# Kernel tuning notes

Hardware: AMD Instinct MI355X
Metric: run time of the kernel (lower is better)

## Reference

```python
import jax, jax.numpy as jnp
import numpy as np

N_FFT = 2048
HOP = 512


def _hann(n):
    # scipy.signal.get_window('hann', n, fftbins=True)
    return (0.5 - 0.5 * np.cos(2.0 * np.pi * np.arange(n) / n)).astype(np.float32)


def setup_inputs() -> dict:
    key = jax.random.key(0)
    k1, k2 = jax.random.split(key)
    B, T, F = 8, 1000, N_FFT // 2 + 1
    real_stft = jax.random.normal(k1, (B, 1, T, F), dtype=jnp.float32)
    imag_stft = jax.random.normal(k2, (B, 1, T, F), dtype=jnp.float32)

    # Windowed IDFT matrices, exactly as ISTFT.__init__ builds conv weights.
    n = N_FFT
    x, y = np.meshgrid(np.arange(n), np.arange(n))
    ang = 2.0 * np.pi * ((x * y) % n) / n  # angle of omega**(x*y), omega = exp(2*pi*i/n)
    win = _hann(n)  # win_length == n_fft -> pad_center is a no-op
    W_real = (np.cos(ang) / n * win[:, None]).astype(np.float32)
    W_imag = (np.sin(ang) / n * win[:, None]).astype(np.float32)

    return {
        "real_stft": real_stft,
        "imag_stft": imag_stft,
        "W_real": jnp.asarray(W_real),
        "W_imag": jnp.asarray(W_imag),
        "window": jnp.asarray(win),
        "length": 511488,  # HOP * (n_frames - 1) with n_frames = 1000
    }


def reference(real_stft, imag_stft, W_real, W_imag, window, length):
    n_fft, hop = N_FFT, HOP
    B = real_stft.shape[0]

    fr = jnp.swapaxes(real_stft[:, 0], 1, 2)  # (B, n_fft//2+1, T)
    fi = jnp.swapaxes(imag_stft[:, 0], 1, 2)
    # Hermitian symmetry -> full (B, n_fft, T) spectrum
    full_r = jnp.concatenate([fr, jnp.flip(fr[:, 1:-1, :], axis=1)], axis=1)
    full_i = jnp.concatenate([fi, -jnp.flip(fi[:, 1:-1, :], axis=1)], axis=1)

    # center=True and length given (static Python int)
    padded_length = length + n_fft
    n_frames = min(fr.shape[2], -(-padded_length // hop))

    # windowed real IFFT per frame: s[b, o, t]
    s = (jnp.einsum('oi,bit->bot', W_real, full_r[:, :, :n_frames])
         - jnp.einsum('oi,bit->bot', W_imag, full_i[:, :, :n_frames]))

    L = n_fft + hop * (n_frames - 1)
    # fused overlap-add via scatter-add
    idx = (jnp.arange(n_frames)[:, None] * hop + jnp.arange(n_fft)[None, :]).reshape(-1)
    frames = jnp.swapaxes(s, 1, 2).reshape(B, -1)  # (B, n_frames*n_fft)
    y = jnp.zeros((B, L), s.dtype).at[:, idx].add(frames)

    # window sum-square normalization (librosa.filters.window_sumsquare)
    wss = jnp.zeros((L,), window.dtype).at[idx].add(jnp.tile(window ** 2, n_frames))
    tiny = jnp.finfo(window.dtype).tiny
    nz = wss > tiny
    y = jnp.where(nz[None, :], y / jnp.where(nz, wss, 1.0)[None, :], y)

    start = n_fft // 2
    return y[:, start:start + length]
```

## Files before the change

### kernel.cpp

```cpp
#include <hip/hip_runtime.h>


#define N_FFT    2048
#define HOP      512
#define T_FRAMES 1000
#define F_BINS   1025
#define OUT_LEN  511488

#define P(a) ((a) + ((a) >> 4))

__device__ __forceinline__ void cmul(float ar, float ai, float br, float bi,
                                     float& cr, float& ci) {
    cr = ar * br - ai * bi;
    ci = ar * bi + ai * br;
}

__device__ __forceinline__ unsigned short f2bf(float f) {
    union { float f; unsigned int u; } v; v.f = f;
    unsigned int u = v.u;
    u += 0x7fffu + ((u >> 16) & 1u);
    return (unsigned short)(u >> 16);
}

__device__ __forceinline__ float bf2f(unsigned short h) {
    union { unsigned int u; float f; } v;
    v.u = ((unsigned int)h) << 16;
    return v.f;
}

__global__ __launch_bounds__(256) void istft_fft_kernel(const float* __restrict__ re,
                                                        const float* __restrict__ im,
                                                        const float* __restrict__ win,
                                                        unsigned short* __restrict__ S) {
    __shared__ float2 buf[1088];

    const int f   = blockIdx.x;
    const int tid = threadIdx.x;
    const float* fr = re + (size_t)f * F_BINS;
    const float* fi = im + (size_t)f * F_BINS;

    const float Sc = 0.5f / 1024.f;
    #pragma unroll
    for (int k0 = 0; k0 < 1024; k0 += 256) {
        int k = k0 + tid;
        float ar = fr[k];
        float ai = (k == 0) ? 0.f : fi[k];
        int mk = 1024 - k;
        float br = fr[mk];
        float bi = (mk == 1024) ? 0.f : fi[mk];
        float dr = ar - br, di = ai + bi;
        float ang = 3.14159265358979f * (float)k / 1024.f;
        float sn, cs;
        __sincosf(ang, &sn, &cs);
        float Zr = (ar + br - (cs * di + sn * dr)) * Sc;
        float Zi = (ai - bi + (cs * dr - sn * di)) * Sc;
        unsigned r10 = __brev((unsigned)k) >> 22;
        int rk = (int)(((r10 & 0x155u) << 1) | ((r10 >> 1) & 0x155u));
        buf[P(rk)] = make_float2(Zr, Zi);
    }
    __syncthreads();

    {
        int base = tid << 2;
        int i0 = P(base), i1 = P(base + 1), i2 = P(base + 2), i3 = P(base + 3);
        float2 a = buf[i0], b = buf[i1], c = buf[i2], d = buf[i3];
        float t0r = a.x + c.x, t0i = a.y + c.y;
        float t1r = a.x - c.x, t1i = a.y - c.y;
        float t2r = b.x + d.x, t2i = b.y + d.y;
        float t3r = b.x - d.x, t3i = b.y - d.y;
        buf[i0] = make_float2(t0r + t2r, t0i + t2i);
        buf[i1] = make_float2(t1r - t3i, t1i + t3r);
        buf[i2] = make_float2(t0r - t2r, t0i - t2i);
        buf[i3] = make_float2(t1r + t3i, t1i - t3r);
    }

    #pragma unroll
    for (int s = 1; s < 4; ++s) {
        __builtin_amdgcn_wave_barrier();
        const int hm = 1 << (2 * s);
        const int j    = tid & (hm - 1);
        const int base = ((tid - j) << 2) + j;
        float ang = 1.57079632679f * (float)j / (float)hm;
        float s1, c1;
        __sincosf(ang, &s1, &c1);
        float c2, s2, c3, s3;
        cmul(c1, s1, c1, s1, c2, s2);
        cmul(c2, s2, c1, s1, c3, s3);

        int i0 = P(base), i1 = P(base + hm), i2 = P(base + 2 * hm), i3 = P(base + 3 * hm);
        float2 a = buf[i0], b = buf[i1], c = buf[i2], d = buf[i3];
        float br_, bi_, cr_, ci_, dr_, di_;
        cmul(b.x, b.y, c1, s1, br_, bi_);
        cmul(c.x, c.y, c2, s2, cr_, ci_);
        cmul(d.x, d.y, c3, s3, dr_, di_);

        float t0r = a.x + cr_, t0i = a.y + ci_;
        float t1r = a.x - cr_, t1i = a.y - ci_;
        float t2r = br_ + dr_, t2i = bi_ + di_;
        float t3r = br_ - dr_, t3i = bi_ - di_;
        buf[i0] = make_float2(t0r + t2r, t0i + t2i);
        buf[i1] = make_float2(t1r - t3i, t1i + t3r);
        buf[i2] = make_float2(t0r - t2r, t0i - t2i);
        buf[i3] = make_float2(t1r + t3i, t1i - t3r);
    }
    __syncthreads();

    {
        unsigned int* dst = (unsigned int*)(S + (size_t)f * N_FFT);
        const float2* w2v = (const float2*)win;

        float ang = 1.57079632679f * (float)tid / 256.f;
        float s1, c1;
        __sincosf(ang, &s1, &c1);
        float c2, s2, c3, s3;
        cmul(c1, s1, c1, s1, c2, s2);
        cmul(c2, s2, c1, s1, c3, s3);

        int i0 = P(tid), i1 = P(tid + 256), i2 = P(tid + 512), i3 = P(tid + 768);
        float2 a = buf[i0], b = buf[i1], c = buf[i2], d = buf[i3];
        float br_, bi_, cr_, ci_, dr_, di_;
        cmul(b.x, b.y, c1, s1, br_, bi_);
        cmul(c.x, c.y, c2, s2, cr_, ci_);
        cmul(d.x, d.y, c3, s3, dr_, di_);

        float t0r = a.x + cr_, t0i = a.y + ci_;
        float t1r = a.x - cr_, t1i = a.y - ci_;
        float t2r = br_ + dr_, t2i = bi_ + di_;
        float t3r = br_ - dr_, t3i = bi_ - di_;

        float2 z0 = make_float2(t0r + t2r, t0i + t2i);
        float2 z1 = make_float2(t1r - t3i, t1i + t3r);
        float2 z2 = make_float2(t0r - t2r, t0i - t2i);
        float2 z3 = make_float2(t1r + t3i, t1i - t3r);

        float2 w0 = w2v[tid],       w1 = w2v[tid + 256];
        float2 w2 = w2v[tid + 512], w3 = w2v[tid + 768];
        dst[tid]       = (unsigned int)f2bf(z0.x * w0.x) | ((unsigned int)f2bf(z0.y * w0.y) << 16);
        dst[tid + 256] = (unsigned int)f2bf(z1.x * w1.x) | ((unsigned int)f2bf(z1.y * w1.y) << 16);
        dst[tid + 512] = (unsigned int)f2bf(z2.x * w2.x) | ((unsigned int)f2bf(z2.y * w2.y) << 16);
        dst[tid + 768] = (unsigned int)f2bf(z3.x * w3.x) | ((unsigned int)f2bf(z3.y * w3.y) << 16);
    }
}

__global__ __launch_bounds__(256) void norm_kernel(const unsigned short* __restrict__ S,
                                                   const float* __restrict__ win,
                                                   float* __restrict__ out) {
    const int b  = blockIdx.y;
    const int m0 = (blockIdx.x * 256 + threadIdx.x) * 8;

    if (blockIdx.x >= 1 && blockIdx.x <= 248) {
        const int n0  = m0 + N_FFT / 2;
        const int thi = n0 >> 9;
        const int r   = n0 & 511;

        float acc[8] = {0.f, 0.f, 0.f, 0.f, 0.f, 0.f, 0.f, 0.f};
        #pragma unroll
        for (int kk = 0; kk < 4; ++kk) {
            const int t = thi - kk;
            const int o = r + (kk << 9);
            const uint4 v = *reinterpret_cast<const uint4*>(
                S + ((size_t)(b * T_FRAMES + t)) * N_FFT + o);
            const unsigned int u[4] = {v.x, v.y, v.z, v.w};
            #pragma unroll
            for (int q = 0; q < 4; ++q) {
                union { unsigned int u32; float f; } lo, hi;
                lo.u32 = u[q] << 16;
                hi.u32 = u[q] & 0xffff0000u;
                acc[2 * q]     += lo.f;
                acc[2 * q + 1] += hi.f;
            }
        }
        const float inv = 1.f / 1.5f;
        float* o_ptr = out + (size_t)b * OUT_LEN + m0;
        float4 v0 = make_float4(acc[0] * inv, acc[1] * inv, acc[2] * inv, acc[3] * inv);
        float4 v1 = make_float4(acc[4] * inv, acc[5] * inv, acc[6] * inv, acc[7] * inv);
        reinterpret_cast<float4*>(o_ptr)[0] = v0;
        reinterpret_cast<float4*>(o_ptr)[1] = v1;
    } else {
        for (int e = 0; e < 8; ++e) {
            int m = m0 + e;
            if (m >= OUT_LEN) continue;
            int n = m + N_FFT / 2;
            int thi = n >> 9; if (thi > T_FRAMES - 1) thi = T_FRAMES - 1;
            int tlo = (n - (N_FFT - HOP)) >> 9; if (tlo < 0) tlo = 0;

            float sum = 0.f, wss = 0.f;
            for (int t = tlo; t <= thi; ++t) {
                int o = n - (t << 9);
                sum += bf2f(S[((size_t)(b * T_FRAMES + t)) * N_FFT + o]);
                float w = win[o];
                wss += w * w;
            }
            out[(size_t)b * OUT_LEN + m] = (wss > 1.17549435e-38f) ? sum / wss : sum;
        }
    }
}

extern "C" void kernel_launch(void* const* d_in, const int* in_sizes, int n_in,
                              void* d_out, int out_size, void* d_ws, size_t ws_size,
                              hipStream_t stream) {
    const float* re  = (const float*)d_in[0];
    const float* im  = (const float*)d_in[1];
    const float* win = (const float*)d_in[4];
    float* out = (float*)d_out;

    unsigned short* S = (unsigned short*)d_ws;

    istft_fft_kernel<<<8000, 256, 0, stream>>>(re, im, win, S);
    norm_kernel<<<dim3(250, 8), 256, 0, stream>>>(S, win, out);
}
```

Baseline: 146.1 us.

## Fuse per-frame IFFT with shared-memory overlap-add and handle block seams separately

Each block now processes eight consecutive frames of one batch item. It accumulates their windowed IFFT outputs in shared memory and writes interior output samples directly, already normalized. Only the overlapping edge regions go to a small fp32 scratch buffer, which a seam kernel sums and normalizes, including the boundary window-sum-square handling. This removes the large bf16 intermediate frame buffer and its global write and read-back. The cost is far fewer blocks, 1000 instead of 8000, with frames handled serially inside each block and extra barriers, so less latency hiding.

```diff
diff --git a/kernel.cpp b/kernel.cpp
--- a/kernel.cpp
+++ b/kernel.cpp
@@ -6,6 +6,9 @@
 #define T_FRAMES 1000
 #define F_BINS   1025
 #define OUT_LEN  511488
+#define FPB      8
+#define BPB      125
+#define OAF      5632
 
 #define P(a) ((a) + ((a) >> 4))
 
@@ -15,184 +18,198 @@
     ci = ar * bi + ai * br;
 }
 
-__device__ __forceinline__ unsigned short f2bf(float f) {
-    union { float f; unsigned int u; } v; v.f = f;
-    unsigned int u = v.u;
-    u += 0x7fffu + ((u >> 16) & 1u);
-    return (unsigned short)(u >> 16);
-}
-
-__device__ __forceinline__ float bf2f(unsigned short h) {
-    union { unsigned int u; float f; } v;
-    v.u = ((unsigned int)h) << 16;
-    return v.f;
-}
-
-__global__ __launch_bounds__(256) void istft_fft_kernel(const float* __restrict__ re,
-                                                        const float* __restrict__ im,
-                                                        const float* __restrict__ win,
-                                                        unsigned short* __restrict__ S) {
-    __shared__ float2 buf[1088];
-
-    const int f   = blockIdx.x;
+__global__ __launch_bounds__(256) void istft_oa_kernel(const float* __restrict__ re,
+                                                       const float* __restrict__ im,
+                                                       const float* __restrict__ win,
+                                                       float* __restrict__ scratch,
+                                                       float* __restrict__ out) {
+    __shared__ __align__(16) float2 buf[1088];
+    __shared__ __align__(16) float2 oa2[OAF / 2];
+
+    const int j   = blockIdx.x;
+    const int b   = blockIdx.y;
     const int tid = threadIdx.x;
-    const float* fr = re + (size_t)f * F_BINS;
-    const float* fi = im + (size_t)f * F_BINS;
+    const int t0  = j * FPB;
+
+    {
+        float4* z4 = (float4*)oa2;
+        #pragma unroll
+        for (int e = 0; e < 6; ++e) {
+            int idx = tid + 256 * e;
+            if (idx < 1408) z4[idx] = make_float4(0.f, 0.f, 0.f, 0.f);
+        }
+    }
 
     const float Sc = 0.5f / 1024.f;
+    const float2* w2v = (const float2*)win;
+
+    for (int d = 0; d < FPB; ++d) {
+        const int f = b * T_FRAMES + t0 + d;
+        const float* fr = re + (size_t)f * F_BINS;
+        const float* fi = im + (size_t)f * F_BINS;
+
+        #pragma unroll
+        for (int k0 = 0; k0 < 1024; k0 += 256) {
+            int k = k0 + tid;
+            float ar = fr[k];
+            float ai = (k == 0) ? 0.f : fi[k];
+            int mk = 1024 - k;
+            float br = fr[mk];
+            float bi = (mk == 1024) ? 0.f : fi[mk];
+            float dr = ar - br, di = ai + bi;
+            float ang = 3.14159265358979f * (float)k / 1024.f;
+            float sn, cs;
+            __sincosf(ang, &sn, &cs);
+            float Zr = (ar + br - (cs * di + sn * dr)) * Sc;
+            float Zi = (ai - bi + (cs * dr - sn * di)) * Sc;
+            unsigned r10 = __brev((unsigned)k) >> 22;
+            int rk = (int)(((r10 & 0x155u) << 1) | ((r10 >> 1) & 0x155u));
+            buf[P(rk)] = make_float2(Zr, Zi);
+        }
+        __syncthreads();
+
+        {
+            int base = tid << 2;
+            int i0 = P(base), i1 = P(base + 1), i2 = P(base + 2), i3 = P(base + 3);
+            float2 a = buf[i0], bb = buf[i1], c = buf[i2], dd = buf[i3];
+            float t0r = a.x + c.x,  t0i = a.y + c.y;
+            float t1r = a.x - c.x,  t1i = a.y - c.y;
+            float t2r = bb.x + dd.x, t2i = bb.y + dd.y;
+            float t3r = bb.x - dd.x, t3i = bb.y - dd.y;
+            buf[i0] = make_float2(t0r + t2r, t0i + t2i);
+            buf[i1] = make_float2(t1r - t3i, t1i + t3r);
+            buf[i2] = make_float2(t0r - t2r, t0i - t2i);
+            buf[i3] = make_float2(t1r + t3i, t1i - t3r);
+        }
+
+        #pragma unroll
+        for (int s = 1; s < 4; ++s) {
+            __builtin_amdgcn_wave_barrier();
+            const int hm = 1 << (2 * s);
+            const int jj   = tid & (hm - 1);
+            const int base = ((tid - jj) << 2) + jj;
+            float ang = 1.57079632679f * (float)jj / (float)hm;
+            float s1, c1;
+            __sincosf(ang, &s1, &c1);
+            float c2, s2, c3, s3;
+            cmul(c1, s1, c1, s1, c2, s2);
+            cmul(c2, s2, c1, s1, c3, s3);
+
+            int i0 = P(base), i1 = P(base + hm), i2 = P(base + 2 * hm), i3 = P(base + 3 * hm);
+            float2 a = buf[i0], bb = buf[i1], c = buf[i2], dd = buf[i3];
+            float br_, bi_, cr_, ci_, dr_, di_;
+            cmul(bb.x, bb.y, c1, s1, br_, bi_);
+            cmul(c.x,  c.y,  c2, s2, cr_, ci_);
+            cmul(dd.x, dd.y, c3, s3, dr_, di_);
+
+            float t0r = a.x + cr_, t0i = a.y + ci_;
+            float t1r = a.x - cr_, t1i = a.y - ci_;
+            float t2r = br_ + dr_, t2i = bi_ + di_;
+            float t3r = br_ - dr_, t3i = bi_ - di_;
+            buf[i0] = make_float2(t0r + t2r, t0i + t2i);
+            buf[i1] = make_float2(t1r - t3i, t1i + t3r);
+            buf[i2] = make_float2(t0r - t2r, t0i - t2i);
+            buf[i3] = make_float2(t1r + t3i, t1i - t3r);
+        }
+        __syncthreads();
+
+        {
+            float ang = 1.57079632679f * (float)tid / 256.f;
+            float s1, c1;
+            __sincosf(ang, &s1, &c1);
+            float c2, s2, c3, s3;
+            cmul(c1, s1, c1, s1, c2, s2);
+            cmul(c2, s2, c1, s1, c3, s3);
+
+            int i0 = P(tid), i1 = P(tid + 256), i2 = P(tid + 512), i3 = P(tid + 768);
+            float2 a = buf[i0], bb = buf[i1], c = buf[i2], dd = buf[i3];
+            float br_, bi_, cr_, ci_, dr_, di_;
+            cmul(bb.x, bb.y, c1, s1, br_, bi_);
+            cmul(c.x,  c.y,  c2, s2, cr_, ci_);
+            cmul(dd.x, dd.y, c3, s3, dr_, di_);
+
+            float t0r = a.x + cr_, t0i = a.y + ci_;
+            float t1r = a.x - cr_, t1i = a.y - ci_;
+            float t2r = br_ + dr_, t2i = bi_ + di_;
+            float t3r = br_ - dr_, t3i = bi_ - di_;
+
+            float2 z0 = make_float2(t0r + t2r, t0i + t2i);
+            float2 z1 = make_float2(t1r - t3i, t1i + t3r);
+            float2 z2 = make_float2(t0r - t2r, t0i - t2i);
+            float2 z3 = make_float2(t1r + t3i, t1i - t3r);
+
+            float2 w0 = w2v[tid],       w1 = w2v[tid + 256];
+            float2 w2 = w2v[tid + 512], w3 = w2v[tid + 768];
+
+            const int base2 = 256 * d;
+            float2 v;
+            v = oa2[base2 + tid];
+            v.x += z0.x * w0.x;  v.y += z0.y * w0.y;
+            oa2[base2 + tid] = v;
+            v = oa2[base2 + tid + 256];
+            v.x += z1.x * w1.x;  v.y += z1.y * w1.y;
+            oa2[base2 + tid + 256] = v;
+            v = oa2[base2 + tid + 512];
+            v.x += z2.x * w2.x;  v.y += z2.y * w2.y;
+            oa2[base2 + tid + 512] = v;
+            v = oa2[base2 + tid + 768];
+            v.x += z3.x * w3.x;  v.y += z3.y * w3.y;
+            oa2[base2 + tid + 768] = v;
+        }
+        __syncthreads();
+    }
+
+    const float inv = 2.f / 3.f;
+    const float4* oa4 = (const float4*)oa2;
+    float4* o4 = (float4*)(out + (size_t)b * OUT_LEN + (size_t)4096 * j + 512);
     #pragma unroll
-    for (int k0 = 0; k0 < 1024; k0 += 256) {
-        int k = k0 + tid;
-        float ar = fr[k];
-        float ai = (k == 0) ? 0.f : fi[k];
-        int mk = 1024 - k;
-        float br = fr[mk];
-        float bi = (mk == 1024) ? 0.f : fi[mk];
-        float dr = ar - br, di = ai + bi;
-        float ang = 3.14159265358979f * (float)k / 1024.f;
-        float sn, cs;
-        __sincosf(ang, &sn, &cs);
-        float Zr = (ar + br - (cs * di + sn * dr)) * Sc;
-        float Zi = (ai - bi + (cs * dr - sn * di)) * Sc;
-        unsigned r10 = __brev((unsigned)k) >> 22;
-        int rk = (int)(((r10 & 0x155u) << 1) | ((r10 >> 1) & 0x155u));
-        buf[P(rk)] = make_float2(Zr, Zi);
-    }
-    __syncthreads();
-
-    {
-        int base = tid << 2;
-        int i0 = P(base), i1 = P(base + 1), i2 = P(base + 2), i3 = P(base + 3);
-        float2 a = buf[i0], b = buf[i1], c = buf[i2], d = buf[i3];
-        float t0r = a.x + c.x, t0i = a.y + c.y;
-        float t1r = a.x - c.x, t1i = a.y - c.y;
-        float t2r = b.x + d.x, t2i = b.y + d.y;
-        float t3r = b.x - d.x, t3i = b.y - d.y;
-        buf[i0] = make_float2(t0r + t2r, t0i + t2i);
-        buf[i1] = make_float2(t1r - t3i, t1i + t3r);
-        buf[i2] = make_float2(t0r - t2r, t0i - t2i);
-        buf[i3] = make_float2(t1r + t3i, t1i - t3r);
-    }
-
+    for (int e = 0; e < 3; ++e) {
+        int idx = tid + 256 * e;
+        if (idx < 640) {
+            float4 v = oa4[384 + idx];
+            o4[idx] = make_float4(v.x * inv, v.y * inv, v.z * inv, v.w * inv);
+        }
+    }
+    float4* sc4 = (float4*)(scratch + (((size_t)b * BPB + j) * 2) * 1536);
     #pragma unroll
-    for (int s = 1; s < 4; ++s) {
-        __builtin_amdgcn_wave_barrier();
-        const int hm = 1 << (2 * s);
-        const int j    = tid & (hm - 1);
-        const int base = ((tid - j) << 2) + j;
-        float ang = 1.57079632679f * (float)j / (float)hm;
-        float s1, c1;
-        __sincosf(ang, &s1, &c1);
-        float c2, s2, c3, s3;
-        cmul(c1, s1, c1, s1, c2, s2);
-        cmul(c2, s2, c1, s1, c3, s3);
-
-        int i0 = P(base), i1 = P(base + hm), i2 = P(base + 2 * hm), i3 = P(base + 3 * hm);
-        float2 a = buf[i0], b = buf[i1], c = buf[i2], d = buf[i3];
-        float br_, bi_, cr_, ci_, dr_, di_;
-        cmul(b.x, b.y, c1, s1, br_, bi_);
-        cmul(c.x, c.y, c2, s2, cr_, ci_);
-        cmul(d.x, d.y, c3, s3, dr_, di_);
-
-        float t0r = a.x + cr_, t0i = a.y + ci_;
-        float t1r = a.x - cr_, t1i = a.y - ci_;
-        float t2r = br_ + dr_, t2i = bi_ + di_;
-        float t3r = br_ - dr_, t3i = bi_ - di_;
-        buf[i0] = make_float2(t0r + t2r, t0i + t2i);
-        buf[i1] = make_float2(t1r - t3i, t1i + t3r);
-        buf[i2] = make_float2(t0r - t2r, t0i - t2i);
-        buf[i3] = make_float2(t1r + t3i, t1i - t3r);
-    }
-    __syncthreads();
-
-    {
-        unsigned int* dst = (unsigned int*)(S + (size_t)f * N_FFT);
-        const float2* w2v = (const float2*)win;
-
-        float ang = 1.57079632679f * (float)tid / 256.f;
-        float s1, c1;
-        __sincosf(ang, &s1, &c1);
-        float c2, s2, c3, s3;
-        cmul(c1, s1, c1, s1, c2, s2);
-        cmul(c2, s2, c1, s1, c3, s3);
-
-        int i0 = P(tid), i1 = P(tid + 256), i2 = P(tid + 512), i3 = P(tid + 768);
-        float2 a = buf[i0], b = buf[i1], c = buf[i2], d = buf[i3];
-        float br_, bi_, cr_, ci_, dr_, di_;
-        cmul(b.x, b.y, c1, s1, br_, bi_);
-        cmul(c.x, c.y, c2, s2, cr_, ci_);
-        cmul(d.x, d.y, c3, s3, dr_, di_);
-
-        float t0r = a.x + cr_, t0i = a.y + ci_;
-        float t1r = a.x - cr_, t1i = a.y - ci_;
-        float t2r = br_ + dr_, t2i = bi_ + di_;
-        float t3r = br_ - dr_, t3i = bi_ - di_;
-
-        float2 z0 = make_float2(t0r + t2r, t0i + t2i);
-        float2 z1 = make_float2(t1r - t3i, t1i + t3r);
-        float2 z2 = make_float2(t0r - t2r, t0i - t2i);
-        float2 z3 = make_float2(t1r + t3i, t1i - t3r);
-
-        float2 w0 = w2v[tid],       w1 = w2v[tid + 256];
-        float2 w2 = w2v[tid + 512], w3 = w2v[tid + 768];
-        dst[tid]       = (unsigned int)f2bf(z0.x * w0.x) | ((unsigned int)f2bf(z0.y * w0.y) << 16);
-        dst[tid + 256] = (unsigned int)f2bf(z1.x * w1.x) | ((unsigned int)f2bf(z1.y * w1.y) << 16);
-        dst[tid + 512] = (unsigned int)f2bf(z2.x * w2.x) | ((unsigned int)f2bf(z2.y * w2.y) << 16);
-        dst[tid + 768] = (unsigned int)f2bf(z3.x * w3.x) | ((unsigned int)f2bf(z3.y * w3.y) << 16);
-    }
-}
-
-__global__ __launch_bounds__(256) void norm_kernel(const unsigned short* __restrict__ S,
+    for (int e = 0; e < 3; ++e) {
+        int idx = tid + 256 * e;
+        float4 v = (idx < 384) ? oa4[idx] : oa4[640 + idx];
+        sc4[idx] = v;
+    }
+}
+
+__global__ __launch_bounds__(256) void seam_kernel(const float* __restrict__ scratch,
                                                    const float* __restrict__ win,
                                                    float* __restrict__ out) {
-    const int b  = blockIdx.y;
-    const int m0 = (blockIdx.x * 256 + threadIdx.x) * 8;
-
-    if (blockIdx.x >= 1 && blockIdx.x <= 248) {
-        const int n0  = m0 + N_FFT / 2;
-        const int thi = n0 >> 9;
-        const int r   = n0 & 511;
-
-        float acc[8] = {0.f, 0.f, 0.f, 0.f, 0.f, 0.f, 0.f, 0.f};
-        #pragma unroll
-        for (int kk = 0; kk < 4; ++kk) {
-            const int t = thi - kk;
-            const int o = r + (kk << 9);
-            const uint4 v = *reinterpret_cast<const uint4*>(
-                S + ((size_t)(b * T_FRAMES + t)) * N_FFT + o);
-            const unsigned int u[4] = {v.x, v.y, v.z, v.w};
-            #pragma unroll
-            for (int q = 0; q < 4; ++q) {
-                union { unsigned int u32; float f; } lo, hi;
-                lo.u32 = u[q] << 16;
-                hi.u32 = u[q] & 0xffff0000u;
-                acc[2 * q]     += lo.f;
-                acc[2 * q + 1] += hi.f;
-            }
-        }
-        const float inv = 1.f / 1.5f;
-        float* o_ptr = out + (size_t)b * OUT_LEN + m0;
-        float4 v0 = make_float4(acc[0] * inv, acc[1] * inv, acc[2] * inv, acc[3] * inv);
-        float4 v1 = make_float4(acc[4] * inv, acc[5] * inv, acc[6] * inv, acc[7] * inv);
-        reinterpret_cast<float4*>(o_ptr)[0] = v0;
-        reinterpret_cast<float4*>(o_ptr)[1] = v1;
-    } else {
-        for (int e = 0; e < 8; ++e) {
-            int m = m0 + e;
-            if (m >= OUT_LEN) continue;
-            int n = m + N_FFT / 2;
+    const int g = blockIdx.x;
+    const int b = blockIdx.y;
+
+    #pragma unroll
+    for (int e = 0; e < 6; ++e) {
+        int i = threadIdx.x + 256 * e;
+        int n = 4096 * g + i;
+        int m = n - 1024;
+        if (m < 0 || m >= OUT_LEN) continue;
+        float s = 0.f;
+        if (g > 0)
+            s += scratch[(((size_t)b * BPB + (g - 1)) * 2 + 1) * 1536 + i];
+        if (g < BPB)
+            s += scratch[(((size_t)b * BPB + g) * 2) * 1536 + i];
+        float r;
+        if (n >= 1536 && n < 512000) {
+            r = s * (2.f / 3.f);
+        } else {
             int thi = n >> 9; if (thi > T_FRAMES - 1) thi = T_FRAMES - 1;
             int tlo = (n - (N_FFT - HOP)) >> 9; if (tlo < 0) tlo = 0;
-
-            float sum = 0.f, wss = 0.f;
+            float wss = 0.f;
             for (int t = tlo; t <= thi; ++t) {
-                int o = n - (t << 9);
-                sum += bf2f(S[((size_t)(b * T_FRAMES + t)) * N_FFT + o]);
-                float w = win[o];
+                float w = win[n - (t << 9)];
                 wss += w * w;
             }
-            out[(size_t)b * OUT_LEN + m] = (wss > 1.17549435e-38f) ? sum / wss : sum;
-        }
+            r = (wss > 1.17549435e-38f) ? s / wss : s;
+        }
+        out[(size_t)b * OUT_LEN + m] = r;
     }
 }
 
@@ -204,8 +221,8 @@
     const float* win = (const float*)d_in[4];
     float* out = (float*)d_out;
 
-    unsigned short* S = (unsigned short*)d_ws;
-
-    istft_fft_kernel<<<8000, 256, 0, stream>>>(re, im, win, S);
-    norm_kernel<<<dim3(250, 8), 256, 0, stream>>>(S, win, out);
-}
+    float* scratch = (float*)d_ws;
+
+    istft_oa_kernel<<<dim3(BPB, 8), 256, 0, stream>>>(re, im, win, scratch, out);
+    seam_kernel<<<dim3(BPB + 1, 8), 256, 0, stream>>>(scratch, win, out);
+}
```

New measurement: 148.7 us. No clear change (+1.8%).
